# Optimization experiments

Measured on AMD Instinct MI355X. Metric: run time of the kernel, lower is better.

The kernel has to match this reference:

```python
import jax, jax.numpy as jnp
import numpy as np

NUM_EMBEDDINGS = 4096
EMBEDDING_DIM = 256
COMMITMENT_COST = 0.25
N_TOKENS = 32768


def setup_inputs() -> dict:
    key = jax.random.key(0)
    k1, k2 = jax.random.split(key)
    inputs = jax.random.normal(k1, (N_TOKENS, EMBEDDING_DIM), dtype=jnp.float32)
    # torch init: uniform(-1/K, 1/K)
    lim = 1.0 / NUM_EMBEDDINGS
    weight = jax.random.uniform(k2, (NUM_EMBEDDINGS, EMBEDDING_DIM), dtype=jnp.float32,
                                minval=-lim, maxval=lim)
    return {"inputs": inputs, "weight": weight}


def reference(inputs, weight):
    distances = (jnp.sum(inputs ** 2, axis=1, keepdims=True)
                 + jnp.sum(weight ** 2, axis=1)
                 - 2.0 * jnp.matmul(inputs, weight.T))
    encoding_indices = jnp.argmin(distances, axis=1)                       # [N]
    encodings = jax.nn.one_hot(encoding_indices, NUM_EMBEDDINGS,
                               dtype=jnp.float32)                          # [N, K]
    # gather replaces onehot @ weight (same values)
    quantized = weight[encoding_indices]                                   # [N, D]

    commitment_loss = jnp.mean((jax.lax.stop_gradient(quantized) - inputs) ** 2)
    codebook_loss = jnp.mean((quantized - jax.lax.stop_gradient(inputs)) ** 2)
    loss = codebook_loss + COMMITMENT_COST * commitment_loss

    # straight-through estimator
    quantized_st = inputs + jax.lax.stop_gradient(quantized - inputs)

    avg_probs = jnp.mean(encodings, axis=0)                                # [K]
    perplexity = jnp.exp(-jnp.sum(avg_probs * jnp.log(avg_probs + 1e-10)))

    return (quantized_st, perplexity, encodings, encoding_indices, loss)
```

## Files before the change

### kernel.cpp

```cpp
#include <hip/hip_runtime.h>

#define N_TOK 32768
#define N_EMB 4096
#define DIM 256

typedef short bf16x8 __attribute__((ext_vector_type(8)));
typedef float f32x4 __attribute__((ext_vector_type(4)));
typedef unsigned short us8 __attribute__((ext_vector_type(8)));


static __device__ __forceinline__ unsigned short f2bf(float f) {
    unsigned int u = __float_as_uint(f);
    u = (u + 0x7fffu + ((u >> 16) & 1u)) >> 16;
    return (unsigned short)u;
}

__device__ __forceinline__ float pw128_sq(const float4* a4) {
#pragma clang fp contract(off)
    float4 v0 = a4[0], v1 = a4[1];
    float r0 = v0.x * v0.x, r1 = v0.y * v0.y, r2 = v0.z * v0.z, r3 = v0.w * v0.w;
    float r4 = v1.x * v1.x, r5 = v1.y * v1.y, r6 = v1.z * v1.z, r7 = v1.w * v1.w;
    #pragma unroll
    for (int i = 1; i < 16; ++i) {
        v0 = a4[2 * i]; v1 = a4[2 * i + 1];
        float s;
        s = v0.x * v0.x; r0 += s;
        s = v0.y * v0.y; r1 += s;
        s = v0.z * v0.z; r2 += s;
        s = v0.w * v0.w; r3 += s;
        s = v1.x * v1.x; r4 += s;
        s = v1.y * v1.y; r5 += s;
        s = v1.z * v1.z; r6 += s;
        s = v1.w * v1.w; r7 += s;
    }
    return ((r0 + r1) + (r2 + r3)) + ((r4 + r5) + (r6 + r7));
}

__global__ __launch_bounds__(256) void k_norm_np(const float* __restrict__ src,
                                                 float* __restrict__ dst, int nrows) {
#pragma clang fp contract(off)
    int row = blockIdx.x * 256 + threadIdx.x;
    if (row >= nrows) return;
    const float4* a = (const float4*)(src + (size_t)row * DIM);
    float lo = pw128_sq(a);
    float hi = pw128_sq(a + 32);
    dst[row] = lo + hi;
}

__global__ __launch_bounds__(256) void k_shuf1(const float* __restrict__ src,
                                               unsigned short* __restrict__ hi) {
    int tid = blockIdx.x * 256 + threadIdx.x;
    int b = tid >> 6, lane = tid & 63;
    int T = b >> 3, C = b & 7;
    int row = T * 16 + (lane & 15);
    int col = C * 32 + (lane >> 4) * 8;
    const float* s = src + (size_t)row * DIM + col;
    us8 h;
    #pragma unroll
    for (int j = 0; j < 8; ++j) h[j] = f2bf(s[j]);
    *(us8*)(hi + (size_t)tid * 8) = h;
}

__global__ __launch_bounds__(256, 4) void k_score_mfma(
        const float* __restrict__ x, const float* __restrict__ w,
        const float* __restrict__ e2_np, const float* __restrict__ x2_np,
        const unsigned short* __restrict__ Xh,
        const unsigned short* __restrict__ Wh,
        float* __restrict__ out_idx, unsigned int* __restrict__ counts,
        float* enc,
        float* __restrict__ outq, float* __restrict__ loss_acc) {
    __shared__ __align__(16) short Abuf[8192];
    __shared__ float Tmax[4][32];
    __shared__ unsigned int ccnt[32];
    __shared__ int clist[32][16];
    __shared__ float Red_d[32 * 8];
    __shared__ int   Red_i[32 * 8];
    __shared__ float sred[4];

    const int t = threadIdx.x;
    const int wave = t >> 6, lane = t & 63;
    const int tok0 = blockIdx.x * 32;
    const int q = lane >> 4, c = lane & 15;

    #pragma unroll
    for (int i = 0; i < 4; ++i) {
        int idx = wave * 4 + i;
        int tile = idx >> 3, C = idx & 7;
        int Tg = blockIdx.x * 2 + tile;
        const unsigned short* src = Xh + ((size_t)(Tg * 8 + C) * 64 + lane) * 8;
        __builtin_amdgcn_global_load_lds(
            (const __attribute__((address_space(1))) unsigned int*)src,
            (__attribute__((address_space(3))) unsigned int*)(Abuf + idx * 512),
            16, 0, 0);
    }
    if (t < 32) ccnt[t] = 0;
    __syncthreads();

    f32x4* ez = enc ? (f32x4*)(enc + (size_t)tok0 * N_EMB) : (f32x4*)0;
    const f32x4 zf4 = {0.f, 0.f, 0.f, 0.f};

    float vmax[8];
    #pragma unroll
    for (int s = 0; s < 8; ++s) vmax[s] = -3.4e38f;
    for (int jt = 0; jt < N_EMB; jt += 256) {
        const int U0 = (jt >> 4) + wave * 4;
        f32x4 acc[2][4] = {};
        #pragma unroll
        for (int C = 0; C < 8; ++C) {
            bf16x8 ah[2], bh[4];
            #pragma unroll
            for (int m = 0; m < 2; ++m)
                ah[m] = *(const bf16x8*)(Abuf + (size_t)(m * 8 + C) * 512 + lane * 8);
            #pragma unroll
            for (int n = 0; n < 4; ++n)
                bh[n] = *(const bf16x8*)(Wh + (((size_t)(U0 + n) * 8 + C) * 64 + lane) * 8);
            #pragma unroll
            for (int m = 0; m < 2; ++m)
                #pragma unroll
                for (int n = 0; n < 4; ++n)
                    acc[m][n] = __builtin_amdgcn_mfma_f32_16x16x32_bf16(ah[m], bh[n], acc[m][n], 0, 0, 0);
        }
        #pragma unroll
        for (int m = 0; m < 2; ++m)
            #pragma unroll
            for (int n = 0; n < 4; ++n)
                #pragma unroll
                for (int r = 0; r < 4; ++r)
                    vmax[m * 4 + r] = fmaxf(vmax[m * 4 + r], acc[m][n][r]);
        if (ez) {
            int base = (jt >> 8) * 8 * 256 + t;
            #pragma unroll
            for (int j = 0; j < 8; ++j)
                __builtin_nontemporal_store(zf4, ez + base + j * 256);
        }
    }
    #pragma unroll
    for (int off = 1; off < 16; off <<= 1)
        #pragma unroll
        for (int s = 0; s < 8; ++s)
            vmax[s] = fmaxf(vmax[s], __shfl_xor(vmax[s], off));
    if (c == 0) {
        #pragma unroll
        for (int m = 0; m < 2; ++m)
            #pragma unroll
            for (int r = 0; r < 4; ++r)
                Tmax[wave][m * 16 + q * 4 + r] = vmax[m * 4 + r];
    }
    __syncthreads();
    if (t < 32) {
        float mx = fmaxf(fmaxf(Tmax[0][t], Tmax[1][t]),
                         fmaxf(Tmax[2][t], Tmax[3][t]));
        Tmax[0][t] = mx - 1.5e-4f;
    }
    __syncthreads();
    float thr[8];
    #pragma unroll
    for (int m = 0; m < 2; ++m)
        #pragma unroll
        for (int r = 0; r < 4; ++r)
            thr[m * 4 + r] = Tmax[0][m * 16 + q * 4 + r];

    for (int jt = 0; jt < N_EMB; jt += 256) {
        const int U0 = (jt >> 4) + wave * 4;
        f32x4 acc[2][4] = {};
        #pragma unroll
        for (int C = 0; C < 8; ++C) {
            bf16x8 ah[2], bh[4];
            #pragma unroll
            for (int m = 0; m < 2; ++m)
                ah[m] = *(const bf16x8*)(Abuf + (size_t)(m * 8 + C) * 512 + lane * 8);
            #pragma unroll
            for (int n = 0; n < 4; ++n)
                bh[n] = *(const bf16x8*)(Wh + (((size_t)(U0 + n) * 8 + C) * 64 + lane) * 8);
            #pragma unroll
            for (int m = 0; m < 2; ++m)
                #pragma unroll
                for (int n = 0; n < 4; ++n)
                    acc[m][n] = __builtin_amdgcn_mfma_f32_16x16x32_bf16(ah[m], bh[n], acc[m][n], 0, 0, 0);
        }
        #pragma unroll
        for (int m = 0; m < 2; ++m)
            #pragma unroll
            for (int n = 0; n < 4; ++n)
                #pragma unroll
                for (int r = 0; r < 4; ++r)
                    if (acc[m][n][r] >= thr[m * 4 + r]) {
                        int tokl = m * 16 + q * 4 + r;
                        int code = (U0 + n) * 16 + c;
                        unsigned int p = atomicAdd(&ccnt[tokl], 1u);
                        if (p < 16) clist[tokl][p] = code;
                    }
    }
    __syncthreads();

    {
        int token = t >> 3, slot = t & 7;
        int cnt = (int)ccnt[token]; if (cnt > 16) cnt = 16;
        float bd = 3.4e38f;
        int bi = 0x7fffffff;
        float x2 = x2_np[tok0 + token];
        const float4* xr = (const float4*)(x + (size_t)(tok0 + token) * DIM);
        for (int k = slot; k < cnt; k += 8) {
            int code = clist[token][k];
            const float4* wr = (const float4*)(w + (size_t)code * DIM);
            double dot = 0.0;
            for (int g = 0; g < 64; ++g) {
                float4 xv = xr[g];
                float4 wv = wr[g];
                dot += (double)xv.x * (double)wv.x;
                dot += (double)xv.y * (double)wv.y;
                dot += (double)xv.z * (double)wv.z;
                dot += (double)xv.w * (double)wv.w;
            }
            {
#pragma clang fp contract(off)
                float M  = (float)dot;
                float S  = x2 + e2_np[code];
                float dd = S - 2.0f * M;
                if (dd < bd || (dd == bd && code < bi)) { bd = dd; bi = code; }
            }
        }
        Red_d[token * 8 + slot] = bd;
        Red_i[token * 8 + slot] = bi;
    }
    __syncthreads();
    if (t < 32) {
        float fv = Red_d[t * 8];
        int   fi = Red_i[t * 8];
        #pragma unroll
        for (int k = 1; k < 8; ++k) {
            float v = Red_d[t * 8 + k];
            int  ii = Red_i[t * 8 + k];
            if (v < fv || (v == fv && ii < fi)) { fv = v; fi = ii; }
        }
        out_idx[tok0 + t] = (float)fi;
        atomicAdd(&counts[fi], 1u);
        ccnt[t] = (unsigned int)fi;
    }
    __syncthreads();

    {
        int token = t >> 3, slot = t & 7;
        int fi = (int)ccnt[token];
        if (enc && slot == 0)
            __builtin_nontemporal_store(1.0f, enc + (size_t)(tok0 + token) * N_EMB + fi);
        const f32x4* wr = (const f32x4*)(w + (size_t)fi * DIM);
        const f32x4* xr = (const f32x4*)(x + (size_t)(tok0 + token) * DIM);
        f32x4* oq = (f32x4*)(outq + (size_t)(tok0 + token) * DIM);
        float sse = 0.f;
        #pragma unroll
        for (int g0 = 0; g0 < 8; ++g0) {
            int g = slot * 8 + g0;
            f32x4 qv = wr[g];
            f32x4 xv = xr[g];
            __builtin_nontemporal_store(qv, oq + g);
            float dx = qv.x - xv.x, dy = qv.y - xv.y;
            float dz = qv.z - xv.z, dw = qv.w - xv.w;
            sse += dx * dx + dy * dy + dz * dz + dw * dw;
        }
        #pragma unroll
        for (int off = 32; off > 0; off >>= 1) sse += __shfl_down(sse, off, 64);
        if (lane == 0) sred[wave] = sse;
    }
    __syncthreads();
    if (t == 0)
        atomicAdd(loss_acc, sred[0] + sred[1] + sred[2] + sred[3]);
}

__global__ __launch_bounds__(256) void k_onehot(const float* __restrict__ out_idx,
                                                float* __restrict__ enc) {
    int token = blockIdx.x;
    int idx = (int)out_idx[token];
    float4* row = (float4*)(enc + (size_t)token * N_EMB);
    #pragma unroll
    for (int p = 0; p < 4; ++p) {
        int g = threadIdx.x + 256 * p;
        float4 v = make_float4(0.f, 0.f, 0.f, 0.f);
        int d0 = g * 4;
        if (idx >= d0 && idx < d0 + 4) ((float*)&v)[idx - d0] = 1.0f;
        row[g] = v;
    }
}

__global__ __launch_bounds__(256) void k_final(const unsigned int* __restrict__ counts,
                                               const float* __restrict__ loss_acc,
                                               float* __restrict__ out_perp,
                                               float* __restrict__ out_loss) {
    __shared__ float sred[4];
    int t = threadIdx.x;
    float h = 0.f;
    for (int k = t; k < N_EMB; k += 256) {
        float p = (float)counts[k] * (1.0f / N_TOK);
        h += p * logf(p + 1e-10f);
    }
    #pragma unroll
    for (int off = 32; off > 0; off >>= 1) h += __shfl_down(h, off, 64);
    if ((t & 63) == 0) sred[t >> 6] = h;
    __syncthreads();
    if (t == 0) {
        float s = sred[0] + sred[1] + sred[2] + sred[3];
        *out_perp = expf(-s);
        *out_loss = loss_acc[0] * 1.25f / 8388608.0f;
    }
}

extern "C" void kernel_launch(void* const* d_in, const int* in_sizes, int n_in,
                              void* d_out, int out_size, void* d_ws, size_t ws_size,
                              hipStream_t stream) {
    const float* x = (const float*)d_in[0];
    const float* w = (const float*)d_in[1];
    float* out  = (float*)d_out;
    float* out0 = out;
    float* out1 = out0 + 8388608;
    float* out2 = out1 + 1;
    float* out3 = out2 + 134217728;
    float* out4 = out3 + 32768;

    unsigned int* counts = (unsigned int*)d_ws;
    float* loss_acc = (float*)((char*)d_ws + 16384);
    float* e2_np    = (float*)((char*)d_ws + 16896);
    float* x2_np    = (float*)((char*)d_ws + 33280);

    bool big_ws = ws_size >= (size_t)(20u * 1024u * 1024u);
    unsigned short *Xh, *Wh;
    float* enc_arg;
    if (big_ws) {
        Xh = (unsigned short*)((char*)d_ws + (1u << 20));
        Wh = Xh + 8388608;
        enc_arg = out2;
    } else {
        uintptr_t sb = ((uintptr_t)out2 + 255) & ~(uintptr_t)255;
        Xh = (unsigned short*)sb;
        Wh = Xh + 8388608;
        enc_arg = nullptr;
    }

    hipMemsetAsync(d_ws, 0, 16640, stream);
    k_norm_np<<<N_EMB / 256, 256, 0, stream>>>(w, e2_np, N_EMB);
    k_norm_np<<<N_TOK / 256, 256, 0, stream>>>(x, x2_np, N_TOK);
    k_shuf1<<<N_TOK * DIM / 8 / 256, 256, 0, stream>>>(x, Xh);
    k_shuf1<<<N_EMB * DIM / 8 / 256, 256, 0, stream>>>(w, Wh);
    k_score_mfma<<<N_TOK / 32, 256, 0, stream>>>(x, w, e2_np, x2_np, Xh, Wh,
                                                 out3, counts, enc_arg,
                                                 out0, loss_acc);
    if (!big_ws)
        k_onehot<<<N_TOK, 256, 0, stream>>>(out3, out2);
    k_final<<<1, 256, 0, stream>>>(counts, loss_acc, out1, out4);
}
```

Measured before the change: 846.6 us.

## Track top-2 candidates per lane to eliminate second GEMM pass

Instead of recomputing the full bf16 distance GEMM in a second pass to collect candidates above the threshold, each lane now keeps its top two scores, with the code index packed into the low 6 mantissa bits. Only these two candidates per lane are checked against the threshold. This halves the MFMA work and weight reads. The risk is that candidates are lost when more than two near-ties fall in the same lane, and that bit-packing perturbs the scores slightly.

```diff
diff --git a/kernel.cpp b/kernel.cpp
--- a/kernel.cpp
+++ b/kernel.cpp
@@ -99,9 +99,9 @@
     f32x4* ez = enc ? (f32x4*)(enc + (size_t)tok0 * N_EMB) : (f32x4*)0;
     const f32x4 zf4 = {0.f, 0.f, 0.f, 0.f};
 
-    float vmax[8];
-    #pragma unroll
-    for (int s = 0; s < 8; ++s) vmax[s] = -3.4e38f;
+    float vmax[8], v2[8];
+    #pragma unroll
+    for (int s = 0; s < 8; ++s) { vmax[s] = -3.4e38f; v2[s] = -3.4e38f; }
     for (int jt = 0; jt < N_EMB; jt += 256) {
         const int U0 = (jt >> 4) + wave * 4;
         f32x4 acc[2][4] = {};
@@ -120,13 +120,21 @@
                 for (int n = 0; n < 4; ++n)
                     acc[m][n] = __builtin_amdgcn_mfma_f32_16x16x32_bf16(ah[m], bh[n], acc[m][n], 0, 0, 0);
         }
-        #pragma unroll
-        for (int m = 0; m < 2; ++m)
-            #pragma unroll
-            for (int n = 0; n < 4; ++n)
+        {
+            unsigned int idb = ((unsigned int)jt >> 8) << 2;
+            #pragma unroll
+            for (int m = 0; m < 2; ++m)
                 #pragma unroll
-                for (int r = 0; r < 4; ++r)
-                    vmax[m * 4 + r] = fmaxf(vmax[m * 4 + r], acc[m][n][r]);
+                for (int n = 0; n < 4; ++n)
+                    #pragma unroll
+                    for (int r = 0; r < 4; ++r) {
+                        float p = __uint_as_float(
+                            (__float_as_uint(acc[m][n][r]) & ~63u) | (idb + (unsigned)n));
+                        int s = m * 4 + r;
+                        if (p > vmax[s]) { v2[s] = vmax[s]; vmax[s] = p; }
+                        else if (p > v2[s]) v2[s] = p;
+                    }
+        }
         if (ez) {
             int base = (jt >> 8) * 8 * 256 + t;
             #pragma unroll
@@ -134,17 +142,20 @@
                 __builtin_nontemporal_store(zf4, ez + base + j * 256);
         }
     }
+    float rmax[8];
+    #pragma unroll
+    for (int s = 0; s < 8; ++s) rmax[s] = vmax[s];
     #pragma unroll
     for (int off = 1; off < 16; off <<= 1)
         #pragma unroll
         for (int s = 0; s < 8; ++s)
-            vmax[s] = fmaxf(vmax[s], __shfl_xor(vmax[s], off));
+            rmax[s] = fmaxf(rmax[s], __shfl_xor(rmax[s], off));
     if (c == 0) {
         #pragma unroll
         for (int m = 0; m < 2; ++m)
             #pragma unroll
             for (int r = 0; r < 4; ++r)
-                Tmax[wave][m * 16 + q * 4 + r] = vmax[m * 4 + r];
+                Tmax[wave][m * 16 + q * 4 + r] = rmax[m * 4 + r];
     }
     __syncthreads();
     if (t < 32) {
@@ -160,36 +171,20 @@
         for (int r = 0; r < 4; ++r)
             thr[m * 4 + r] = Tmax[0][m * 16 + q * 4 + r];
 
-    for (int jt = 0; jt < N_EMB; jt += 256) {
-        const int U0 = (jt >> 4) + wave * 4;
-        f32x4 acc[2][4] = {};
-        #pragma unroll
-        for (int C = 0; C < 8; ++C) {
-            bf16x8 ah[2], bh[4];
-            #pragma unroll
-            for (int m = 0; m < 2; ++m)
-                ah[m] = *(const bf16x8*)(Abuf + (size_t)(m * 8 + C) * 512 + lane * 8);
-            #pragma unroll
-            for (int n = 0; n < 4; ++n)
-                bh[n] = *(const bf16x8*)(Wh + (((size_t)(U0 + n) * 8 + C) * 64 + lane) * 8);
-            #pragma unroll
-            for (int m = 0; m < 2; ++m)
-                #pragma unroll
-                for (int n = 0; n < 4; ++n)
-                    acc[m][n] = __builtin_amdgcn_mfma_f32_16x16x32_bf16(ah[m], bh[n], acc[m][n], 0, 0, 0);
-        }
-        #pragma unroll
-        for (int m = 0; m < 2; ++m)
-            #pragma unroll
-            for (int n = 0; n < 4; ++n)
-                #pragma unroll
-                for (int r = 0; r < 4; ++r)
-                    if (acc[m][n][r] >= thr[m * 4 + r]) {
-                        int tokl = m * 16 + q * 4 + r;
-                        int code = (U0 + n) * 16 + c;
-                        unsigned int p = atomicAdd(&ccnt[tokl], 1u);
-                        if (p < 16) clist[tokl][p] = code;
-                    }
+    #pragma unroll
+    for (int s = 0; s < 8; ++s) {
+        int m = s >> 2, r = s & 3;
+        int tokl = m * 16 + q * 4 + r;
+        #pragma unroll
+        for (int h = 0; h < 2; ++h) {
+            float pv = h ? v2[s] : vmax[s];
+            if (pv >= thr[s]) {
+                unsigned int id = __float_as_uint(pv) & 63u;
+                int code = ((int)(id >> 2) * 16 + wave * 4 + (int)(id & 3u)) * 16 + c;
+                unsigned int p = atomicAdd(&ccnt[tokl], 1u);
+                if (p < 16) clist[tokl][p] = code;
+            }
+        }
     }
     __syncthreads();
 
```

Result: faster. 756.5 us (-10.6%).
